# Optimization experiments

Hardware: AMD Instinct MI355X
Metric: run time of the kernel (lower is better)

The kernel has to match this reference:

```python
import jax, jax.numpy as jnp
import numpy as np

N = 50000; E = 1000000; H = 64; HEADS = 4; D = 16; IN = 8; ED = 4; B = 512; EMB = 128; L = 3


def _ln(x, g, b, eps=1e-5):
    mu = jnp.mean(x, axis=-1, keepdims=True)
    var = jnp.mean((x - mu) ** 2, axis=-1, keepdims=True)
    return (x - mu) / jnp.sqrt(var + eps) * g + b


def setup_inputs() -> dict:
    key = jax.random.key(0)
    ks = jax.random.split(key, 24)
    rn = lambda k, s, sc=0.05: jax.random.normal(k, s, jnp.float32) * sc
    return {
        'x': rn(ks[0], (N, IN), 1.0),
        'edge_attr': rn(ks[1], (E, ED), 1.0),
        'edge_index': jax.random.randint(ks[2], (2, E), 0, N),
        'batch': jnp.sort(jax.random.randint(ks[3], (N,), 0, B)),
        'W_in': rn(ks[4], (IN, H)), 'b_in': jnp.zeros(H, jnp.float32),
        'ln1_g': jnp.ones((L, H), jnp.float32), 'ln1_b': jnp.zeros((L, H), jnp.float32),
        'Wq': rn(ks[5], (L, H, H)), 'bq': jnp.zeros((L, H), jnp.float32),
        'Wk': rn(ks[6], (L, H, H)), 'bk': jnp.zeros((L, H), jnp.float32),
        'Wv': rn(ks[7], (L, H, H)), 'bv': jnp.zeros((L, H), jnp.float32),
        'We': rn(ks[8], (L, ED, H)),
        'Wskip': rn(ks[9], (L, H, H)), 'bskip': jnp.zeros((L, H), jnp.float32),
        'Wbeta': rn(ks[10], (L, 3 * H, 1)),
        'ln2_g': jnp.ones((L, H), jnp.float32), 'ln2_b': jnp.zeros((L, H), jnp.float32),
        'W1': rn(ks[11], (L, H, 2 * H)), 'b1': jnp.zeros((L, 2 * H), jnp.float32),
        'W2': rn(ks[12], (L, 2 * H, H)), 'b2': jnp.zeros((L, H), jnp.float32),
        'Wo1': rn(ks[13], (H, EMB)), 'bo1': jnp.zeros(EMB, jnp.float32),
        'Wo2': rn(ks[14], (EMB, EMB)), 'bo2': jnp.zeros(EMB, jnp.float32),
    }


def _forward(x, edge_attr, edge_index, batch, W_in, b_in, ln1_g, ln1_b, Wq, bq, Wk, bk, Wv, bv,
             We, Wskip, bskip, Wbeta, ln2_g, ln2_b, W1, b1, W2, b2, Wo1, bo1, Wo2, bo2):
    src, dst = edge_index[0], edge_index[1]  # message j->i aggregated at dst
    scale = 1.0 / jnp.sqrt(jnp.float32(D))
    x = x @ W_in + b_in  # [N,H]
    for l in range(L):
        xin = x
        h = _ln(x, ln1_g[l], ln1_b[l])
        q = (h @ Wq[l] + bq[l]).reshape(N, HEADS, D)
        k = (h @ Wk[l] + bk[l]).reshape(N, HEADS, D)
        v = (h @ Wv[l] + bv[l]).reshape(N, HEADS, D)
        e = (edge_attr @ We[l]).reshape(E, HEADS, D)
        k_e = k[src] + e  # [E,heads,D]
        v_e = v[src] + e
        s = jnp.sum(q[dst] * k_e, axis=-1) * scale  # [E,heads]
        m = jax.ops.segment_max(s, dst, num_segments=N)  # scatter-softmax max
        m = jnp.where(jnp.isfinite(m), m, 0.0)
        p = jnp.exp(s - m[dst])
        denom = jax.ops.segment_sum(p, dst, num_segments=N)
        alpha = p / (denom[dst] + 1e-16)
        out = jax.ops.segment_sum(alpha[:, :, None] * v_e, dst, num_segments=N).reshape(N, H)
        x_r = h @ Wskip[l] + bskip[l]
        beta = jax.nn.sigmoid(jnp.concatenate([out, x_r, out - x_r], axis=-1) @ Wbeta[l])
        out = beta * x_r + (1.0 - beta) * out
        x = xin + out  # dropout disabled (eval)
        xin = x
        h = _ln(x, ln2_g[l], ln2_b[l])
        h = jax.nn.gelu(h @ W1[l] + b1[l], approximate=False) @ W2[l] + b2[l]
        x = xin + h
    pooled = jax.ops.segment_max(x, batch, num_segments=B)  # global_max_pool
    pooled = jnp.where(jnp.isfinite(pooled), pooled, 0.0)
    emb = jax.nn.relu(pooled @ Wo1 + bo1) @ Wo2 + bo2
    norm = jnp.sqrt(jnp.sum(emb * emb, axis=-1, keepdims=True))
    return emb / jnp.maximum(norm, 1e-12)


def reference(x, edge_attr, edge_index, batch, W_in, b_in, ln1_g, ln1_b, Wq, bq, Wk, bk, Wv, bv,
              We, Wskip, bskip, Wbeta, ln2_g, ln2_b, W1, b1, W2, b2, Wo1, bo1, Wo2, bo2):
    return _forward(x, edge_attr, edge_index, batch, W_in, b_in, ln1_g, ln1_b, Wq, bq, Wk, bk,
                    Wv, bv, We, Wskip, bskip, Wbeta, ln2_g, ln2_b, W1, b1, W2, b2, Wo1, bo1, Wo2, bo2)
```

## Files before the change

kernel.cpp:

```cpp
#include <hip/hip_runtime.h>
#include <hip/hip_bf16.h>
#include <hip/hip_fp16.h>

#define Nn 50000
#define Ee 1000000
#define Bb 512
#define NG 3125
#define SCB 196
#define GB 782

typedef unsigned short u16;
typedef unsigned int u32;
typedef _Float16 f16;
typedef _Float16 f16x8 __attribute__((ext_vector_type(8)));
typedef float f32x4 __attribute__((ext_vector_type(4)));

__device__ __forceinline__ u16 f2h(float f) { return __half_as_ushort(__float2half(f)); }
__device__ __forceinline__ float h2f_lo(u32 kv) { return __half2float(__ushort_as_half((u16)(kv & 0xffff))); }
__device__ __forceinline__ float h2f_hi(u32 kv) { return __half2float(__ushort_as_half((u16)(kv >> 16))); }

__device__ __forceinline__ float fexp2(float x) {
    float r;
    asm("v_exp_f32 %0, %1" : "=v"(r) : "v"(x));
    return r;
}

__device__ __forceinline__ float red16(float x) {
    int t;
    t = __builtin_amdgcn_update_dpp(0, __float_as_int(x), 0xB1, 0xF, 0xF, true);
    x += __int_as_float(t);
    t = __builtin_amdgcn_update_dpp(0, __float_as_int(x), 0x4E, 0xF, 0xF, true);
    x += __int_as_float(t);
    t = __builtin_amdgcn_update_dpp(0, __float_as_int(x), 0x141, 0xF, 0xF, true);
    x += __int_as_float(t);
    t = __builtin_amdgcn_update_dpp(0, __float_as_int(x), 0x140, 0xF, 0xF, true);
    x += __int_as_float(t);
    return x;
}

__global__ __launch_bounds__(256) void k_input_proj(const float* __restrict__ x,
    const float* __restrict__ Win, const float* __restrict__ bin, float* __restrict__ X)
{
    __shared__ float W[8][64];
    __shared__ float bsh[64];
    int t = threadIdx.x;
    if (t < 64) bsh[t] = bin[t];
    for (int i = t; i < 512; i += 256) W[i >> 6][i & 63] = Win[i];
    __syncthreads();
    int gid = blockIdx.x * 256 + t;
    int n = gid >> 6, c = gid & 63;
    const float* xr = x + n * 8;
    float acc = bsh[c];
#pragma unroll
    for (int k = 0; k < 8; ++k) acc = fmaf(xr[k], W[k][c], acc);
    X[gid] = acc;
}

__global__ __launch_bounds__(256) void k_hist(const int* __restrict__ ei, int* __restrict__ deg)
{
    int e = blockIdx.x * 256 + threadIdx.x;
    if (e < Ee) atomicAdd(&deg[ei[Ee + e]], 1);
}

__global__ __launch_bounds__(256) void k_part(const int* __restrict__ deg, int* __restrict__ psum)
{
    __shared__ int ws[4];
    int b = blockIdx.x, t = threadIdx.x;
    int idx = b * 256 + t;
    int v = (idx < Nn) ? deg[idx] : 0;
    int r = v;
#pragma unroll
    for (int off = 32; off; off >>= 1) r += __shfl_xor(r, off);
    if ((t & 63) == 0) ws[t >> 6] = r;
    __syncthreads();
    if (t == 0) psum[b] = ws[0] + ws[1] + ws[2] + ws[3];
}

__global__ __launch_bounds__(256) void k_scanp(const int* __restrict__ psum, int* __restrict__ poff)
{
    __shared__ int ws[4];
    int t = threadIdx.x, lane = t & 63, w = t >> 6;
    int v = (t < SCB) ? psum[t] : 0;
    int s = v;
#pragma unroll
    for (int off = 1; off < 64; off <<= 1) {
        int u = __shfl_up(s, off);
        if (lane >= off) s += u;
    }
    if (lane == 63) ws[w] = s;
    __syncthreads();
    if (t == 0) { int a = 0; for (int i = 0; i < 4; ++i) { a += ws[i]; ws[i] = a; } }
    __syncthreads();
    int incl = s + (w ? ws[w - 1] : 0);
    if (t < SCB) poff[t] = incl - v;
}

__global__ __launch_bounds__(256) void k_apply(const int* __restrict__ deg, const int* __restrict__ poff,
    int* __restrict__ rowptr)
{
    __shared__ int ws[4];
    int b = blockIdx.x, t = threadIdx.x, lane = t & 63, w = t >> 6;
    int idx = b * 256 + t;
    int v = (idx < Nn) ? deg[idx] : 0;
    int s = v;
#pragma unroll
    for (int off = 1; off < 64; off <<= 1) {
        int u = __shfl_up(s, off);
        if (lane >= off) s += u;
    }
    if (lane == 63) ws[w] = s;
    __syncthreads();
    if (t == 0) { int a = 0; for (int i = 0; i < 4; ++i) { a += ws[i]; ws[i] = a; } }
    __syncthreads();
    int incl = s + (w ? ws[w - 1] : 0) + poff[b];
    if (idx < Nn) rowptr[idx + 1] = incl;
    if (b == 0 && t == 0) rowptr[0] = 0;
}

__global__ __launch_bounds__(256) void k_scatter(const int* __restrict__ ei, const float* __restrict__ eattr,
    const int* __restrict__ rowptr, int* __restrict__ cursor, int* __restrict__ colsrc,
    float4* __restrict__ ea4)
{
    int e = blockIdx.x * 256 + threadIdx.x;
    if (e >= Ee) return;
    int d = ei[Ee + e];
    int pos = rowptr[d] + atomicAdd(&cursor[d], 1);
    colsrc[pos] = ei[e];
    ea4[pos] = *(const float4*)(eattr + (size_t)e * 4);
}

__device__ __forceinline__ f16x8 load_bfrag(const float* __restrict__ W, int NC, int col, int k0)
{
    f16x8 b;
    const float* wp = W + (size_t)k0 * NC + col;
#pragma unroll
    for (int i = 0; i < 8; ++i) b[i] = (f16)wp[i * NC];
    return b;
}

__device__ __forceinline__ void build_ln_a(const float* __restrict__ X, int n0, int lane,
    const float* __restrict__ lng, const float* __restrict__ lnb, f16x8* a)
{
    const int r = lane & 15, c = lane >> 4;
    const float* xp = X + (size_t)(n0 + r) * 64 + c * 8;
    float4 x0 = *(const float4*)(xp);
    float4 x1 = *(const float4*)(xp + 4);
    float4 x2 = *(const float4*)(xp + 32);
    float4 x3 = *(const float4*)(xp + 36);
    float xs[16] = {x0.x, x0.y, x0.z, x0.w, x1.x, x1.y, x1.z, x1.w,
                    x2.x, x2.y, x2.z, x2.w, x3.x, x3.y, x3.z, x3.w};
    float s = 0.f, s2 = 0.f;
#pragma unroll
    for (int i = 0; i < 16; ++i) { s += xs[i]; s2 = fmaf(xs[i], xs[i], s2); }
    s += __shfl_xor(s, 16);  s += __shfl_xor(s, 32);
    s2 += __shfl_xor(s2, 16); s2 += __shfl_xor(s2, 32);
    float mu = s * 0.015625f;
    float var = s2 * 0.015625f - mu * mu;
    float rstd = rsqrtf(fmaxf(var, 0.f) + 1e-5f);
    const float* gp = lng + c * 8;
    const float* bp = lnb + c * 8;
    float4 g0 = *(const float4*)(gp),      g1 = *(const float4*)(gp + 4);
    float4 g2 = *(const float4*)(gp + 32), g3 = *(const float4*)(gp + 36);
    float4 b0 = *(const float4*)(bp),      b1 = *(const float4*)(bp + 4);
    float4 b2 = *(const float4*)(bp + 32), b3 = *(const float4*)(bp + 36);
    float gs[16] = {g0.x, g0.y, g0.z, g0.w, g1.x, g1.y, g1.z, g1.w,
                    g2.x, g2.y, g2.z, g2.w, g3.x, g3.y, g3.z, g3.w};
    float bs[16] = {b0.x, b0.y, b0.z, b0.w, b1.x, b1.y, b1.z, b1.w,
                    b2.x, b2.y, b2.z, b2.w, b3.x, b3.y, b3.z, b3.w};
#pragma unroll
    for (int i = 0; i < 16; ++i) {
        float h = (xs[i] - mu) * rstd * gs[i] + bs[i];
        a[i >> 3][i & 7] = (f16)h;
    }
}

__global__ __launch_bounds__(256) void k_proj(const float* __restrict__ X,
    float* __restrict__ QX, u32* __restrict__ KV,
    const float* __restrict__ Wq, const float* __restrict__ Ws,
    const float* __restrict__ Wk, const float* __restrict__ Wv,
    const float* __restrict__ bq, const float* __restrict__ bs_,
    const float* __restrict__ bk, const float* __restrict__ bv,
    const float* __restrict__ lng, const float* __restrict__ lnb)
{
    const int lane = threadIdx.x & 63;
    const int wid = (blockIdx.x * 256 + threadIdx.x) >> 6;
    const int nw = gridDim.x * 4;
    const int ch_base = lane & 15;
    const int k0b = (lane >> 4) * 8;
    float bq_l[4], bs_l[4], bk_l[4], bv_l[4];
#pragma unroll
    for (int t = 0; t < 4; ++t) {
        bq_l[t] = bq[t * 16 + ch_base]; bs_l[t] = bs_[t * 16 + ch_base];
        bk_l[t] = bk[t * 16 + ch_base]; bv_l[t] = bv[t * 16 + ch_base];
    }
    for (int g = wid; g < NG; g += nw) {
        int n0 = g * 16;
        f16x8 a[2];
        build_ln_a(X, n0, lane, lng, lnb, a);
        int rbase = n0 + (lane >> 4) * 4;
        {
            f16x8 bw[8][2];
#pragma unroll
            for (int t = 0; t < 4; ++t)
#pragma unroll
                for (int s = 0; s < 2; ++s) {
                    bw[t][s]     = load_bfrag(Wq, 64, t * 16 + ch_base, s * 32 + k0b);
                    bw[t + 4][s] = load_bfrag(Ws, 64, t * 16 + ch_base, s * 32 + k0b);
                }
            f32x4 acc[8];
#pragma unroll
            for (int t = 0; t < 8; ++t) { acc[t][0] = 0.f; acc[t][1] = 0.f; acc[t][2] = 0.f; acc[t][3] = 0.f; }
#pragma unroll
            for (int t = 0; t < 8; ++t)
#pragma unroll
                for (int s = 0; s < 2; ++s)
                    acc[t] = __builtin_amdgcn_mfma_f32_16x16x32_f16(a[s], bw[t][s], acc[t], 0, 0, 0);
#pragma unroll
            for (int t = 0; t < 4; ++t) {
                int ch = t * 16 + ch_base;
#pragma unroll
                for (int j = 0; j < 4; ++j) {
                    float* dst = QX + (size_t)(rbase + j) * 128;
                    dst[ch] = acc[t][j] + bq_l[t];
                    dst[64 + ch] = acc[t + 4][j] + bs_l[t];
                }
            }
        }
        {
            f16x8 bw[8][2];
#pragma unroll
            for (int t = 0; t < 4; ++t)
#pragma unroll
                for (int s = 0; s < 2; ++s) {
                    bw[t][s]     = load_bfrag(Wk, 64, t * 16 + ch_base, s * 32 + k0b);
                    bw[t + 4][s] = load_bfrag(Wv, 64, t * 16 + ch_base, s * 32 + k0b);
                }
            f32x4 acc[8];
#pragma unroll
            for (int t = 0; t < 8; ++t) { acc[t][0] = 0.f; acc[t][1] = 0.f; acc[t][2] = 0.f; acc[t][3] = 0.f; }
#pragma unroll
            for (int t = 0; t < 8; ++t)
#pragma unroll
                for (int s = 0; s < 2; ++s)
                    acc[t] = __builtin_amdgcn_mfma_f32_16x16x32_f16(a[s], bw[t][s], acc[t], 0, 0, 0);
#pragma unroll
            for (int t = 0; t < 4; ++t) {
                int ch = t * 16 + ch_base;
#pragma unroll
                for (int j = 0; j < 4; ++j) {
                    u32 lo = f2h(acc[t][j] + bk_l[t]);
                    u32 hi = f2h(acc[t + 4][j] + bv_l[t]);
                    KV[(size_t)(rbase + j) * 64 + ch] = (hi << 16) | lo;
                }
            }
        }
    }
}

__global__ __launch_bounds__(256) void k_edge(
    const float* __restrict__ QX, const u32* __restrict__ KV, float* __restrict__ X,
    const int* __restrict__ rowptr, const int* __restrict__ colsrc,
    const float4* __restrict__ ea4,
    const float* __restrict__ We, const float* __restrict__ Wbeta)
{
    const float SCL = 0.25f * 1.4426950408889634f;
    int lane = threadIdx.x & 63;
    int node = blockIdx.x * 4 + (threadIdx.x >> 6);
    if (node >= Nn) return;
    float we0 = We[lane], we1 = We[64 + lane];
    float we2 = We[128 + lane], we3 = We[192 + lane];
    float wbA = Wbeta[lane] + Wbeta[128 + lane];
    float wbB = Wbeta[64 + lane] - Wbeta[128 + lane];
    const float* qrow = QX + (size_t)node * 128;
    float q = qrow[lane] * SCL;
    float xr = qrow[64 + lane];
    int jb = rowptr[node], je = rowptr[node + 1];
    float l0 = 0.f, l1 = 0.f, a0 = 0.f, a1 = 0.f;
    int j = jb;
    for (; j + 3 < je; j += 4) {
        int src[4]; float4 eb[4]; u32 kv[4];
#pragma unroll
        for (int c = 0; c < 4; ++c) src[c] = colsrc[j + c];
#pragma unroll
        for (int c = 0; c < 4; ++c) kv[c] = KV[(src[c] << 6) | lane];
#pragma unroll
        for (int c = 0; c < 4; ++c) eb[c] = ea4[j + c];
        float pe[4], ve[4];
#pragma unroll
        for (int c = 0; c < 4; ++c) {
            float e = we0 * eb[c].x;
            e = fmaf(we1, eb[c].y, e); e = fmaf(we2, eb[c].z, e); e = fmaf(we3, eb[c].w, e);
            float ke = h2f_lo(kv[c]) + e;
            ve[c] = h2f_hi(kv[c]) + e;
            float p = red16(q * ke);
            pe[c] = fexp2(p);
        }
        l0 += pe[0]; l1 += pe[1];
        a0 = fmaf(pe[0], ve[0], a0); a1 = fmaf(pe[1], ve[1], a1);
        l0 += pe[2]; l1 += pe[3];
        a0 = fmaf(pe[2], ve[2], a0); a1 = fmaf(pe[3], ve[3], a1);
    }
    for (; j < je; ++j) {
        int s0 = colsrc[j];
        float4 eb0 = ea4[j];
        u32 kv0 = KV[(s0 << 6) | lane];
        float e0 = we0 * eb0.x;
        e0 = fmaf(we1, eb0.y, e0); e0 = fmaf(we2, eb0.z, e0); e0 = fmaf(we3, eb0.w, e0);
        float ke0 = h2f_lo(kv0) + e0, ve0 = h2f_hi(kv0) + e0;
        float p0 = red16(q * ke0);
        float pe0 = fexp2(p0);
        l0 += pe0;
        a0 = fmaf(pe0, ve0, a0);
    }
    float lsum = l0 + l1;
    float acc = a0 + a1;
    float outv = acc / (lsum + 1e-16f);
    float tb = outv * wbA + xr * wbB;
#pragma unroll
    for (int off = 32; off; off >>= 1) tb += __shfl_xor(tb, off);
    float beta = 1.f / (1.f + __expf(-tb));
    float res = beta * xr + (1.f - beta) * outv;
    X[(size_t)node * 64 + lane] += res;
}

__global__ __launch_bounds__(256) void k_ffn1_m(const float* __restrict__ X, u16* __restrict__ G16,
    const float* __restrict__ W1, const float* __restrict__ b1,
    const float* __restrict__ lng, const float* __restrict__ lnb)
{
    const int lane = threadIdx.x & 63;
    const int wid = (blockIdx.x * 256 + threadIdx.x) >> 6;
    const int nw = gridDim.x * 4;
    const int ch_base = lane & 15;
    const int k0b = (lane >> 4) * 8;
    f16x8 bw[8][2];
#pragma unroll
    for (int t = 0; t < 8; ++t)
#pragma unroll
        for (int s = 0; s < 2; ++s)
            bw[t][s] = load_bfrag(W1, 128, t * 16 + ch_base, s * 32 + k0b);
    float b1_l[8];
#pragma unroll
    for (int t = 0; t < 8; ++t) b1_l[t] = b1[t * 16 + ch_base];
    for (int g = wid; g < NG; g += nw) {
        int n0 = g * 16;
        f16x8 a[2];
        build_ln_a(X, n0, lane, lng, lnb, a);
        f32x4 acc[8];
#pragma unroll
        for (int t = 0; t < 8; ++t) { acc[t][0] = 0.f; acc[t][1] = 0.f; acc[t][2] = 0.f; acc[t][3] = 0.f; }
#pragma unroll
        for (int t = 0; t < 8; ++t)
#pragma unroll
            for (int s = 0; s < 2; ++s)
                acc[t] = __builtin_amdgcn_mfma_f32_16x16x32_f16(a[s], bw[t][s], acc[t], 0, 0, 0);
        int rbase = n0 + (lane >> 4) * 4;
#pragma unroll
        for (int t = 0; t < 8; ++t) {
            int ch = t * 16 + ch_base;
#pragma unroll
            for (int j = 0; j < 4; ++j) {
                float v = acc[t][j] + b1_l[t];
                float o = 0.5f * v * (1.f + erff(v * 0.7071067811865476f));
                G16[(size_t)(rbase + j) * 128 + ch] = f2h(o);
            }
        }
    }
}

__global__ __launch_bounds__(256) void k_ffn2_m(const u16* __restrict__ G16, float* __restrict__ X,
    const float* __restrict__ W2, const float* __restrict__ b2,
    const int* __restrict__ batch, u32* __restrict__ pkeys, int dopool)
{
    const int lane = threadIdx.x & 63;
    const int wid = (blockIdx.x * 256 + threadIdx.x) >> 6;
    const int nw = gridDim.x * 4;
    const int ch_base = lane & 15;
    const int k0b = (lane >> 4) * 8;
    f16x8 bw[4][4];
#pragma unroll
    for (int t = 0; t < 4; ++t)
#pragma unroll
        for (int s = 0; s < 4; ++s)
            bw[t][s] = load_bfrag(W2, 64, t * 16 + ch_base, s * 32 + k0b);
    float b2_l[4];
#pragma unroll
    for (int t = 0; t < 4; ++t) b2_l[t] = b2[t * 16 + ch_base];
    for (int g = wid; g < NG; g += nw) {
        int n0 = g * 16;
        const u16* gp = G16 + (size_t)(n0 + ch_base) * 128 + k0b;
        f16x8 a0 = *(const f16x8*)(gp);
        f16x8 a1 = *(const f16x8*)(gp + 32);
        f16x8 a2 = *(const f16x8*)(gp + 64);
        f16x8 a3 = *(const f16x8*)(gp + 96);
        f32x4 acc[4];
#pragma unroll
        for (int t = 0; t < 4; ++t) { acc[t][0] = 0.f; acc[t][1] = 0.f; acc[t][2] = 0.f; acc[t][3] = 0.f; }
#pragma unroll
        for (int t = 0; t < 4; ++t) {
            acc[t] = __builtin_amdgcn_mfma_f32_16x16x32_f16(a0, bw[t][0], acc[t], 0, 0, 0);
            acc[t] = __builtin_amdgcn_mfma_f32_16x16x32_f16(a1, bw[t][1], acc[t], 0, 0, 0);
            acc[t] = __builtin_amdgcn_mfma_f32_16x16x32_f16(a2, bw[t][2], acc[t], 0, 0, 0);
            acc[t] = __builtin_amdgcn_mfma_f32_16x16x32_f16(a3, bw[t][3], acc[t], 0, 0, 0);
        }
        int rbase = n0 + (lane >> 4) * 4;
#pragma unroll
        for (int t = 0; t < 4; ++t) {
            int ch = t * 16 + ch_base;
#pragma unroll
            for (int j = 0; j < 4; ++j) {
                int n = rbase + j;
                float* dst = X + (size_t)n * 64 + ch;
                float v = *dst + acc[t][j] + b2_l[t];
                *dst = v;
                if (dopool) {
                    u32 u = __float_as_uint(v);
                    u32 key = (u >> 31) ? ~u : (u | 0x80000000u);
                    atomicMax(&pkeys[batch[n] * 64 + ch], key);
                }
            }
        }
    }
}

__global__ __launch_bounds__(128) void k_head(const u32* __restrict__ pkeys,
    const float* __restrict__ Wo1, const float* __restrict__ bo1,
    const float* __restrict__ Wo2, const float* __restrict__ bo2,
    float* __restrict__ out)
{
    __shared__ float P[64];
    __shared__ float E1[128];
    __shared__ float wred[2];
    int b = blockIdx.x, t = threadIdx.x;
    if (t < 64) {
        u32 k = pkeys[b * 64 + t];
        float v = 0.f;
        if (k) v = (k >> 31) ? __uint_as_float(k ^ 0x80000000u) : __uint_as_float(~k);
        P[t] = v;
    }
    __syncthreads();
    float a = bo1[t];
#pragma unroll 8
    for (int k = 0; k < 64; ++k) a = fmaf(P[k], Wo1[k * 128 + t], a);
    E1[t] = fmaxf(a, 0.f);
    __syncthreads();
    float o = bo2[t];
#pragma unroll 8
    for (int k = 0; k < 128; ++k) o = fmaf(E1[k], Wo2[k * 128 + t], o);
    float ss = o * o;
#pragma unroll
    for (int off = 32; off; off >>= 1) ss += __shfl_xor(ss, off);
    if ((t & 63) == 0) wred[t >> 6] = ss;
    __syncthreads();
    float tot = wred[0] + wred[1];
    float nrm = fmaxf(sqrtf(tot), 1e-12f);
    out[b * 128 + t] = o / nrm;
}

extern "C" void kernel_launch(void* const* d_in, const int* in_sizes, int n_in,
                              void* d_out, int out_size, void* d_ws, size_t ws_size,
                              hipStream_t stream)
{
    const float* x         = (const float*)d_in[0];
    const float* edge_attr = (const float*)d_in[1];
    const int* ei          = (const int*)d_in[2];
    const int* batch       = (const int*)d_in[3];
    const float* Win  = (const float*)d_in[4];
    const float* bin  = (const float*)d_in[5];
    const float* ln1g = (const float*)d_in[6];
    const float* ln1b = (const float*)d_in[7];
    const float* Wq   = (const float*)d_in[8];
    const float* bq   = (const float*)d_in[9];
    const float* Wk   = (const float*)d_in[10];
    const float* bk   = (const float*)d_in[11];
    const float* Wv   = (const float*)d_in[12];
    const float* bv   = (const float*)d_in[13];
    const float* We   = (const float*)d_in[14];
    const float* Wsk  = (const float*)d_in[15];
    const float* bsk  = (const float*)d_in[16];
    const float* Wbe  = (const float*)d_in[17];
    const float* ln2g = (const float*)d_in[18];
    const float* ln2b = (const float*)d_in[19];
    const float* W1   = (const float*)d_in[20];
    const float* b1   = (const float*)d_in[21];
    const float* W2   = (const float*)d_in[22];
    const float* b2   = (const float*)d_in[23];
    const float* Wo1  = (const float*)d_in[24];
    const float* bo1  = (const float*)d_in[25];
    const float* Wo2  = (const float*)d_in[26];
    const float* bo2  = (const float*)d_in[27];

    char* wsp = (char*)d_ws;
    size_t off = 0;
    auto alloc = [&](size_t bytes) { void* p = wsp + off; off = (off + bytes + 255) & ~(size_t)255; return p; };
    float*   X      = (float*)alloc((size_t)Nn * 64 * 4);
    float*   QX     = (float*)alloc((size_t)Nn * 128 * 4);
    u32*     KV     = (u32*)alloc((size_t)Nn * 64 * 4);
    u16*     G16    = (u16*)alloc((size_t)Nn * 128 * 2);
    int*     rowptr = (int*)alloc((size_t)(Nn + 1) * 4);
    int*     deg    = (int*)alloc((size_t)Nn * 4);
    int*     cursor = (int*)alloc((size_t)Nn * 4);
    int*     psum   = (int*)alloc((size_t)SCB * 4);
    int*     poff   = (int*)alloc((size_t)SCB * 4);
    int*     colsrc = (int*)alloc((size_t)Ee * 4);
    float4*  ea4    = (float4*)alloc((size_t)Ee * 16);
    u32*     pkeys  = (u32*)alloc((size_t)Bb * 64 * 4);

    hipMemsetAsync(deg, 0, (size_t)Nn * 4, stream);
    hipMemsetAsync(cursor, 0, (size_t)Nn * 4, stream);
    hipMemsetAsync(pkeys, 0, (size_t)Bb * 64 * 4, stream);

    k_input_proj<<<12500, 256, 0, stream>>>(x, Win, bin, X);
    k_hist<<<(Ee + 255) / 256, 256, 0, stream>>>(ei, deg);
    k_part<<<SCB, 256, 0, stream>>>(deg, psum);
    k_scanp<<<1, 256, 0, stream>>>(psum, poff);
    k_apply<<<SCB, 256, 0, stream>>>(deg, poff, rowptr);
    k_scatter<<<(Ee + 255) / 256, 256, 0, stream>>>(ei, edge_attr, rowptr, cursor, colsrc, ea4);

    for (int l = 0; l < 3; ++l) {
        k_proj<<<GB, 256, 0, stream>>>(X, QX, KV,
            Wq + l * 4096, Wsk + l * 4096, Wk + l * 4096, Wv + l * 4096,
            bq + l * 64, bsk + l * 64, bk + l * 64, bv + l * 64,
            ln1g + l * 64, ln1b + l * 64);
        k_edge<<<Nn / 4, 256, 0, stream>>>(QX, KV, X, rowptr, colsrc, ea4,
            We + l * 256, Wbe + l * 192);
        k_ffn1_m<<<GB, 256, 0, stream>>>(X, G16, W1 + l * 8192, b1 + l * 128,
            ln2g + l * 64, ln2b + l * 64);
        k_ffn2_m<<<GB, 256, 0, stream>>>(G16, X, W2 + l * 8192, b2 + l * 64,
            batch, pkeys, (l == 2) ? 1 : 0);
    }
    k_head<<<Bb, 128, 0, stream>>>(pkeys, Wo1, bo1, Wo2, bo2, (float*)d_out);
}
```

Baseline: 482.3 us.

## Pack edge records with fp16 attributes, store Q/skip in fp16, unroll edge loop by 8

Merges the separate colsrc and edge-attribute arrays into one 16-byte record per edge holding the source index and the four attributes packed as fp16. The edge kernel then computes the edge embedding with fdot2. Q and skip projections are now stored as fp16, which halves QX traffic. The edge loop is unrolled by 8 with four accumulators so more gathers are in flight at once. The cost is lower precision for Q, skip and edge attributes, plus higher register pressure from the wider unroll.

New measurement: 437.7 us. 9.2% less time.

```diff
diff --git a/kernel.cpp b/kernel.cpp
--- a/kernel.cpp
+++ b/kernel.cpp
@@ -12,12 +12,16 @@
 typedef unsigned short u16;
 typedef unsigned int u32;
 typedef _Float16 f16;
+typedef _Float16 f16x2 __attribute__((ext_vector_type(2)));
 typedef _Float16 f16x8 __attribute__((ext_vector_type(8)));
 typedef float f32x4 __attribute__((ext_vector_type(4)));
+typedef int i32x4 __attribute__((ext_vector_type(4)));
 
 __device__ __forceinline__ u16 f2h(float f) { return __half_as_ushort(__float2half(f)); }
+__device__ __forceinline__ float h2f(u16 h) { return __half2float(__ushort_as_half(h)); }
 __device__ __forceinline__ float h2f_lo(u32 kv) { return __half2float(__ushort_as_half((u16)(kv & 0xffff))); }
 __device__ __forceinline__ float h2f_hi(u32 kv) { return __half2float(__ushort_as_half((u16)(kv >> 16))); }
+__device__ __forceinline__ f16x2 as_h2(u32 v) { union { u32 u; f16x2 h; } c; c.u = v; return c.h; }
 
 __device__ __forceinline__ float fexp2(float x) {
     float r;
@@ -118,15 +122,19 @@
 }
 
 __global__ __launch_bounds__(256) void k_scatter(const int* __restrict__ ei, const float* __restrict__ eattr,
-    const int* __restrict__ rowptr, int* __restrict__ cursor, int* __restrict__ colsrc,
-    float4* __restrict__ ea4)
+    const int* __restrict__ rowptr, int* __restrict__ cursor, i32x4* __restrict__ EC)
 {
     int e = blockIdx.x * 256 + threadIdx.x;
     if (e >= Ee) return;
     int d = ei[Ee + e];
     int pos = rowptr[d] + atomicAdd(&cursor[d], 1);
-    colsrc[pos] = ei[e];
-    ea4[pos] = *(const float4*)(eattr + (size_t)e * 4);
+    float4 ea = *(const float4*)(eattr + (size_t)e * 4);
+    i32x4 rec;
+    rec[0] = ei[e];
+    rec[1] = (int)(((u32)f2h(ea.y) << 16) | f2h(ea.x));
+    rec[2] = (int)(((u32)f2h(ea.w) << 16) | f2h(ea.z));
+    rec[3] = 0;
+    __builtin_nontemporal_store(rec, EC + pos);
 }
 
 __device__ __forceinline__ f16x8 load_bfrag(const float* __restrict__ W, int NC, int col, int k0)
@@ -175,7 +183,7 @@
 }
 
 __global__ __launch_bounds__(256) void k_proj(const float* __restrict__ X,
-    float* __restrict__ QX, u32* __restrict__ KV,
+    u16* __restrict__ QXh, u32* __restrict__ KV,
     const float* __restrict__ Wq, const float* __restrict__ Ws,
     const float* __restrict__ Wk, const float* __restrict__ Wv,
     const float* __restrict__ bq, const float* __restrict__ bs_,
@@ -220,9 +228,9 @@
                 int ch = t * 16 + ch_base;
 #pragma unroll
                 for (int j = 0; j < 4; ++j) {
-                    float* dst = QX + (size_t)(rbase + j) * 128;
-                    dst[ch] = acc[t][j] + bq_l[t];
-                    dst[64 + ch] = acc[t + 4][j] + bs_l[t];
+                    u16* dst = QXh + (size_t)(rbase + j) * 128;
+                    dst[ch] = f2h(acc[t][j] + bq_l[t]);
+                    dst[64 + ch] = f2h(acc[t + 4][j] + bs_l[t]);
                 }
             }
         }
@@ -258,62 +266,71 @@
 }
 
 __global__ __launch_bounds__(256) void k_edge(
-    const float* __restrict__ QX, const u32* __restrict__ KV, float* __restrict__ X,
-    const int* __restrict__ rowptr, const int* __restrict__ colsrc,
-    const float4* __restrict__ ea4,
+    const u16* __restrict__ QXh, const u32* __restrict__ KV, float* __restrict__ X,
+    const int* __restrict__ rowptr, const i32x4* __restrict__ EC,
     const float* __restrict__ We, const float* __restrict__ Wbeta)
 {
     const float SCL = 0.25f * 1.4426950408889634f;
     int lane = threadIdx.x & 63;
-    int node = blockIdx.x * 4 + (threadIdx.x >> 6);
-    if (node >= Nn) return;
-    float we0 = We[lane], we1 = We[64 + lane];
-    float we2 = We[128 + lane], we3 = We[192 + lane];
+    int node = __builtin_amdgcn_readfirstlane(blockIdx.x * 4 + (threadIdx.x >> 6));
+    f16x2 w01, w23;
+    w01[0] = (f16)We[lane];        w01[1] = (f16)We[64 + lane];
+    w23[0] = (f16)We[128 + lane];  w23[1] = (f16)We[192 + lane];
     float wbA = Wbeta[lane] + Wbeta[128 + lane];
     float wbB = Wbeta[64 + lane] - Wbeta[128 + lane];
-    const float* qrow = QX + (size_t)node * 128;
-    float q = qrow[lane] * SCL;
-    float xr = qrow[64 + lane];
+    const u16* qrow = QXh + (size_t)node * 128;
+    float q = h2f(qrow[lane]) * SCL;
+    float xr = h2f(qrow[64 + lane]);
     int jb = rowptr[node], je = rowptr[node + 1];
-    float l0 = 0.f, l1 = 0.f, a0 = 0.f, a1 = 0.f;
+    float l[4] = {0.f, 0.f, 0.f, 0.f};
+    float a[4] = {0.f, 0.f, 0.f, 0.f};
     int j = jb;
+    for (; j + 7 < je; j += 8) {
+        i32x4 r[8]; u32 kv[8];
+#pragma unroll
+        for (int c = 0; c < 8; ++c) r[c] = EC[j + c];
+#pragma unroll
+        for (int c = 0; c < 8; ++c) kv[c] = KV[(r[c][0] << 6) | lane];
+#pragma unroll
+        for (int c = 0; c < 8; ++c) {
+            float e = __builtin_amdgcn_fdot2(w01, as_h2((u32)r[c][1]),
+                        __builtin_amdgcn_fdot2(w23, as_h2((u32)r[c][2]), 0.f, false), false);
+            float ke = h2f_lo(kv[c]) + e;
+            float ve = h2f_hi(kv[c]) + e;
+            float pe = fexp2(red16(q * ke));
+            l[c & 3] += pe;
+            a[c & 3] = fmaf(pe, ve, a[c & 3]);
+        }
+    }
     for (; j + 3 < je; j += 4) {
-        int src[4]; float4 eb[4]; u32 kv[4];
-#pragma unroll
-        for (int c = 0; c < 4; ++c) src[c] = colsrc[j + c];
-#pragma unroll
-        for (int c = 0; c < 4; ++c) kv[c] = KV[(src[c] << 6) | lane];
-#pragma unroll
-        for (int c = 0; c < 4; ++c) eb[c] = ea4[j + c];
-        float pe[4], ve[4];
+        i32x4 r[4]; u32 kv[4];
+#pragma unroll
+        for (int c = 0; c < 4; ++c) r[c] = EC[j + c];
+#pragma unroll
+        for (int c = 0; c < 4; ++c) kv[c] = KV[(r[c][0] << 6) | lane];
 #pragma unroll
         for (int c = 0; c < 4; ++c) {
-            float e = we0 * eb[c].x;
-            e = fmaf(we1, eb[c].y, e); e = fmaf(we2, eb[c].z, e); e = fmaf(we3, eb[c].w, e);
+            float e = __builtin_amdgcn_fdot2(w01, as_h2((u32)r[c][1]),
+                        __builtin_amdgcn_fdot2(w23, as_h2((u32)r[c][2]), 0.f, false), false);
             float ke = h2f_lo(kv[c]) + e;
-            ve[c] = h2f_hi(kv[c]) + e;
-            float p = red16(q * ke);
-            pe[c] = fexp2(p);
-        }
-        l0 += pe[0]; l1 += pe[1];
-        a0 = fmaf(pe[0], ve[0], a0); a1 = fmaf(pe[1], ve[1], a1);
-        l0 += pe[2]; l1 += pe[3];
-        a0 = fmaf(pe[2], ve[2], a0); a1 = fmaf(pe[3], ve[3], a1);
+            float ve = h2f_hi(kv[c]) + e;
+            float pe = fexp2(red16(q * ke));
+            l[c] += pe;
+            a[c] = fmaf(pe, ve, a[c]);
+        }
     }
     for (; j < je; ++j) {
-        int s0 = colsrc[j];
-        float4 eb0 = ea4[j];
-        u32 kv0 = KV[(s0 << 6) | lane];
-        float e0 = we0 * eb0.x;
-        e0 = fmaf(we1, eb0.y, e0); e0 = fmaf(we2, eb0.z, e0); e0 = fmaf(we3, eb0.w, e0);
+        i32x4 r0 = EC[j];
+        u32 kv0 = KV[(r0[0] << 6) | lane];
+        float e0 = __builtin_amdgcn_fdot2(w01, as_h2((u32)r0[1]),
+                     __builtin_amdgcn_fdot2(w23, as_h2((u32)r0[2]), 0.f, false), false);
         float ke0 = h2f_lo(kv0) + e0, ve0 = h2f_hi(kv0) + e0;
-        float p0 = red16(q * ke0);
-        float pe0 = fexp2(p0);
-        l0 += pe0;
-        a0 = fmaf(pe0, ve0, a0);
-    }
-    float lsum = l0 + l1;
-    float acc = a0 + a1;
+        float pe0 = fexp2(red16(q * ke0));
+        l[0] += pe0;
+        a[0] = fmaf(pe0, ve0, a[0]);
+    }
+    float lsum = (l[0] + l[1]) + (l[2] + l[3]);
+    float acc = (a[0] + a[1]) + (a[2] + a[3]);
     float outv = acc / (lsum + 1e-16f);
     float tb = outv * wbA + xr * wbB;
 #pragma unroll
@@ -493,7 +510,7 @@
     size_t off = 0;
     auto alloc = [&](size_t bytes) { void* p = wsp + off; off = (off + bytes + 255) & ~(size_t)255; return p; };
     float*   X      = (float*)alloc((size_t)Nn * 64 * 4);
-    float*   QX     = (float*)alloc((size_t)Nn * 128 * 4);
+    u16*     QXh    = (u16*)alloc((size_t)Nn * 128 * 2);
     u32*     KV     = (u32*)alloc((size_t)Nn * 64 * 4);
     u16*     G16    = (u16*)alloc((size_t)Nn * 128 * 2);
     int*     rowptr = (int*)alloc((size_t)(Nn + 1) * 4);
@@ -501,8 +518,7 @@
     int*     cursor = (int*)alloc((size_t)Nn * 4);
     int*     psum   = (int*)alloc((size_t)SCB * 4);
     int*     poff   = (int*)alloc((size_t)SCB * 4);
-    int*     colsrc = (int*)alloc((size_t)Ee * 4);
-    float4*  ea4    = (float4*)alloc((size_t)Ee * 16);
+    i32x4*   EC     = (i32x4*)alloc((size_t)Ee * 16);
     u32*     pkeys  = (u32*)alloc((size_t)Bb * 64 * 4);
 
     hipMemsetAsync(deg, 0, (size_t)Nn * 4, stream);
@@ -514,14 +530,14 @@
     k_part<<<SCB, 256, 0, stream>>>(deg, psum);
     k_scanp<<<1, 256, 0, stream>>>(psum, poff);
     k_apply<<<SCB, 256, 0, stream>>>(deg, poff, rowptr);
-    k_scatter<<<(Ee + 255) / 256, 256, 0, stream>>>(ei, edge_attr, rowptr, cursor, colsrc, ea4);
+    k_scatter<<<(Ee + 255) / 256, 256, 0, stream>>>(ei, edge_attr, rowptr, cursor, EC);
 
     for (int l = 0; l < 3; ++l) {
-        k_proj<<<GB, 256, 0, stream>>>(X, QX, KV,
+        k_proj<<<GB, 256, 0, stream>>>(X, QXh, KV,
             Wq + l * 4096, Wsk + l * 4096, Wk + l * 4096, Wv + l * 4096,
             bq + l * 64, bsk + l * 64, bk + l * 64, bv + l * 64,
             ln1g + l * 64, ln1b + l * 64);
-        k_edge<<<Nn / 4, 256, 0, stream>>>(QX, KV, X, rowptr, colsrc, ea4,
+        k_edge<<<Nn / 4, 256, 0, stream>>>(QXh, KV, X, rowptr, EC,
             We + l * 256, Wbe + l * 192);
         k_ffn1_m<<<GB, 256, 0, stream>>>(X, G16, W1 + l * 8192, b1 + l * 128,
             ln2g + l * 64, ln2b + l * 64);
```
